# Kernel tuning notes

Measured on AMD Instinct MI355X. Metric: run time of the kernel, lower is better.

Reference implementation:

```python
import jax, jax.numpy as jnp
import numpy as np

B, LQ, D = 4, 10000, 256
HEADS, LVLS, PTS = 8, 1, 4
HW = 100
LIN = HW * HW


def setup_inputs() -> dict:
    key = jax.random.key(0)
    ks = jax.random.split(key, 14)
    s = 0.02
    ctr = jax.random.uniform(ks[2], (B, LQ, LVLS, 2), jnp.float32)
    wh = 0.05 + 0.2 * jax.random.uniform(ks[3], (B, LQ, LVLS, 2), jnp.float32)
    return {
        "query": jax.random.normal(ks[0], (B, LQ, D), jnp.float32),
        "reference_points": jnp.concatenate([ctr, wh], axis=-1),
        "input_flatten": jax.random.normal(ks[1], (B, LIN, D), jnp.float32),
        "input_spatial_shapes": jnp.array([[HW, HW]], jnp.int32),
        "input_level_start_index": jnp.zeros((LVLS,), jnp.int32),
        "input_padding_mask": jnp.zeros((B, LIN), jnp.bool_),
        "Wv": s * jax.random.normal(ks[4], (D, D), jnp.float32),
        "bv": jnp.zeros((D,), jnp.float32),
        "Woff": s * jax.random.normal(ks[5], (D, HEADS * LVLS * PTS * 2), jnp.float32),
        "boff": s * jax.random.normal(ks[6], (HEADS * LVLS * PTS * 2,), jnp.float32),
        "Wa": s * jax.random.normal(ks[7], (D, HEADS * LVLS * PTS), jnp.float32),
        "ba": jnp.zeros((HEADS * LVLS * PTS,), jnp.float32),
        "Wout": s * jax.random.normal(ks[8], (D, D), jnp.float32),
        "bout": jnp.zeros((D,), jnp.float32),
    }


def _ms_deform_attn(query, reference_points, input_flatten, input_padding_mask,
                    Wv, bv, Woff, boff, Wa, ba, Wout, bout):
    Bn, Lq, Dm = query.shape
    Lin = input_flatten.shape[1]
    Hh, L, P = HEADS, LVLS, PTS
    Cd = Dm // Hh
    # value projection + padding mask
    value = input_flatten @ Wv + bv
    value = jnp.where(input_padding_mask[..., None], 0.0, value)
    # sampling offsets & attention weights
    off = (query @ Woff + boff).reshape(Bn, Lq, Hh, L, P, 2)
    attn = jax.nn.softmax((query @ Wa + ba).reshape(Bn, Lq, Hh, L * P), axis=-1)
    loc = (reference_points[:, :, None, :, None, :2]
           + off / P * reference_points[:, :, None, :, None, 2:] * 0.5)
    # value -> (B*Hh, Cd, Lin); square single-level map H=W=sqrt(Lin)
    v = value.reshape(Bn, Lin, Hh, Cd).transpose(0, 2, 3, 1).reshape(Bn * Hh, Cd, Lin)
    Hs = int(round(Lin ** 0.5)); Ws = Hs
    # level 0 grid: (B*Hh, Lq, P, 2), normalized to [-1, 1]
    g = (2.0 * loc - 1.0)[:, :, :, 0].transpose(0, 2, 1, 3, 4).reshape(Bn * Hh, Lq, P, 2)
    x = (g[..., 0] + 1.0) * Ws / 2.0 - 0.5
    y = (g[..., 1] + 1.0) * Hs / 2.0 - 0.5
    x0 = jnp.floor(x).astype(jnp.int32); y0 = jnp.floor(y).astype(jnp.int32)
    x1 = x0 + 1; y1 = y0 + 1
    wx = x - x0.astype(x.dtype); wy = y - y0.astype(y.dtype)

    def valid(xi, yi):
        return ((xi >= 0) & (xi < Ws) & (yi >= 0) & (yi < Hs)).astype(value.dtype)

    def gather(xi, yi):
        idx = (jnp.clip(yi, 0, Hs - 1) * Ws + jnp.clip(xi, 0, Ws - 1)).reshape(Bn * Hh, 1, Lq * P)
        out = jnp.take_along_axis(v, jnp.broadcast_to(idx, (Bn * Hh, Cd, Lq * P)), axis=2)
        return out.reshape(Bn * Hh, Cd, Lq, P)

    sv = (gather(x0, y0) * ((1 - wx) * (1 - wy) * valid(x0, y0))[:, None]
          + gather(x0, y1) * ((1 - wx) * wy * valid(x0, y1))[:, None]
          + gather(x1, y0) * (wx * (1 - wy) * valid(x1, y0))[:, None]
          + gather(x1, y1) * (wx * wy * valid(x1, y1))[:, None])  # (B*Hh, Cd, Lq, P)
    aw = attn.transpose(0, 2, 1, 3).reshape(Bn * Hh, 1, Lq, L * P)
    out = (sv * aw).sum(-1).reshape(Bn, Hh * Cd, Lq).transpose(0, 2, 1)  # (B, Lq, D)
    return out @ Wout + bout


def reference(query, reference_points, input_flatten, input_spatial_shapes,
              input_level_start_index, input_padding_mask,
              Wv, bv, Woff, boff, Wa, ba, Wout, bout):
    # input_spatial_shapes / level_start_index are redundant here: the core is
    # single-level with H=W=sqrt(Len_in) (faithful to the source code).
    return _ms_deform_attn(query, reference_points, input_flatten, input_padding_mask,
                           Wv, bv, Woff, boff, Wa, ba, Wout, bout)
```

## Files before the change

kernel.cpp:

```cpp
#include <hip/hip_runtime.h>

#define BATCH 4
#define LQ    10000
#define DM    256
#define NH    8
#define NP    4
#define HWD   100
#define LIN   10000

typedef unsigned short ushort_t;
typedef __attribute__((ext_vector_type(8))) short bf16x8;
typedef __attribute__((ext_vector_type(8))) unsigned short u16x8;
typedef __attribute__((ext_vector_type(4))) float f32x4;

__device__ __forceinline__ unsigned short f2bf(float f) {
    unsigned int u = __float_as_uint(f);
    u += 0x7FFFu + ((u >> 16) & 1u);
    return (unsigned short)(u >> 16);
}

__device__ __forceinline__ u16x8 pack8(float4 f0, float4 f1) {
    u16x8 pk;
    pk[0] = f2bf(f0.x); pk[1] = f2bf(f0.y);
    pk[2] = f2bf(f0.z); pk[3] = f2bf(f0.w);
    pk[4] = f2bf(f1.x); pk[5] = f2bf(f1.y);
    pk[6] = f2bf(f1.z); pk[7] = f2bf(f1.w);
    return pk;
}

__device__ __forceinline__ void gload16(const ushort_t* g, ushort_t* l) {
    __builtin_amdgcn_global_load_lds(
        (const __attribute__((address_space(1))) void*)g,
        (__attribute__((address_space(3))) void*)l, 16, 0, 0);
}

__global__ __launch_bounds__(256) void prep_kernel(
    const float* __restrict__ Wv, const float* __restrict__ Wout,
    const float* __restrict__ Woff, const float* __restrict__ Wa,
    const float* __restrict__ boff, const float* __restrict__ ba,
    ushort_t* __restrict__ WtV, ushort_t* __restrict__ WtO,
    ushort_t* __restrict__ Wcomb, float* __restrict__ bcomb)
{
    const int n = blockIdx.x, k = threadIdx.x;
    const int t32 = k >> 5, lc = (k >> 3) & 3, j = k & 7;
    const int ct = lc ^ ((n >> 1) & 3);
    const size_t addr = (size_t)n * 256 + t32 * 32 + ct * 8 + j;
    if (blockIdx.y == 0) {
        WtV[addr] = f2bf(Wv[(size_t)k * 256 + n]);
    } else if (blockIdx.y == 1) {
        WtO[addr] = f2bf(Wout[(size_t)k * 256 + n]);
    } else if (n < 96) {
        float w = (n < 64) ? Woff[(size_t)k * 64 + n] : Wa[(size_t)k * 32 + (n - 64)];
        Wcomb[addr] = f2bf(w);
        if (k == 0) bcomb[n] = (n < 64) ? boff[n] : ba[n - 64];
    }
}

__global__ __launch_bounds__(256) void gemm_in_kernel(
    const float* __restrict__ flat, const float* __restrict__ query,
    const ushort_t* __restrict__ WtV, const ushort_t* __restrict__ Wcomb,
    const float* __restrict__ bv, const float* __restrict__ bcomb,
    ushort_t* __restrict__ value, float* __restrict__ oaproj)
{
    __shared__ ushort_t As[2][64 * 32];
    __shared__ ushort_t Bs[2][128 * 32];

    const int tid  = threadIdx.x;
    const int lane = tid & 63;
    const int wv   = tid >> 6;

    const int ar  = tid >> 2;
    const int akb = tid & 3;
    const int asw = (akb ^ ((ar >> 1) & 3)) * 8;
    const int fr = lane & 15, kb = lane >> 4;
    const int ln4 = lane >> 2, lc4 = lane & 3;

    const bool isVal = (blockIdx.x < 1250);
    const int row0 = isVal ? (blockIdx.x >> 1) * 64 : (blockIdx.x - 1250) * 64;
    const int col0 = isVal ? (blockIdx.x & 1) * 128 : 0;
    const float* ap = isVal ? &flat [(size_t)(row0 + ar) * 256 + akb * 8]
                            : &query[(size_t)(row0 + ar) * 256 + akb * 8];
    const ushort_t* Wt = isVal ? WtV : Wcomb;
    const int nrows = isVal ? 128 : 96;

    const f32x4 zero = {0.f, 0.f, 0.f, 0.f};
    f32x4 acc[4][2];
    #pragma unroll
    for (int m = 0; m < 4; ++m)
        #pragma unroll
        for (int n = 0; n < 2; ++n) acc[m][n] = zero;

    {
        float4 f0 = *reinterpret_cast<const float4*>(ap);
        float4 f1 = *reinterpret_cast<const float4*>(ap + 4);
        #pragma unroll
        for (int it = 0; it < 2; ++it) {
            int r0 = (it * 4 + wv) * 16;
            if (r0 < nrows)
                gload16(&Wt[(size_t)(col0 + r0 + ln4) * 256 + lc4 * 8],
                        &Bs[0][r0 * 32]);
        }
        *reinterpret_cast<u16x8*>(&As[0][ar * 32 + asw]) = pack8(f0, f1);
    }
    __syncthreads();

    int c = 0;
    for (int t = 0; t < 8; ++t) {
        const int kn = (t + 1) * 32;
        const bool pf = (t < 7);
        float4 f0, f1;
        if (pf) {
            f0 = *reinterpret_cast<const float4*>(ap + kn);
            f1 = *reinterpret_cast<const float4*>(ap + kn + 4);
            #pragma unroll
            for (int it = 0; it < 2; ++it) {
                int r0 = (it * 4 + wv) * 16;
                if (r0 < nrows)
                    gload16(&Wt[(size_t)(col0 + r0 + ln4) * 256 + kn + lc4 * 8],
                            &Bs[c ^ 1][r0 * 32]);
            }
        }
        bf16x8 af[4], bf[2];
        #pragma unroll
        for (int m = 0; m < 4; ++m) {
            int r = m * 16 + fr;
            af[m] = *reinterpret_cast<const bf16x8*>(
                &As[c][r * 32 + ((kb ^ ((r >> 1) & 3)) * 8)]);
        }
        #pragma unroll
        for (int n = 0; n < 2; ++n) {
            int lr = wv * 32 + n * 16 + fr;
            bf[n] = *reinterpret_cast<const bf16x8*>(
                &Bs[c][lr * 32 + ((kb ^ ((lr >> 1) & 3)) * 8)]);
        }
        #pragma unroll
        for (int m = 0; m < 4; ++m)
            #pragma unroll
            for (int n = 0; n < 2; ++n)
                acc[m][n] = __builtin_amdgcn_mfma_f32_16x16x32_bf16(
                    af[m], bf[n], acc[m][n], 0, 0, 0);
        if (pf)
            *reinterpret_cast<u16x8*>(&As[c ^ 1][ar * 32 + asw]) = pack8(f0, f1);
        __syncthreads();
        c ^= 1;
    }

    if (isVal) {
        #pragma unroll
        for (int n = 0; n < 2; ++n) {
            int cc = col0 + wv * 32 + n * 16 + fr;
            float bb = bv[cc];
            int hh = cc >> 5, ch = cc & 31;
            #pragma unroll
            for (int m = 0; m < 4; ++m) {
                #pragma unroll
                for (int j = 0; j < 4; ++j) {
                    int r = row0 + m * 16 + kb * 4 + j;
                    int rb = (int)((unsigned)r / 10000u);
                    int pix = r - rb * 10000;
                    size_t addr = (((size_t)(rb * 8 + hh)) * LIN + pix) * 32 + ch;
                    value[addr] = f2bf(acc[m][n][j] + bb);
                }
            }
        }
    } else {
        #pragma unroll
        for (int n = 0; n < 2; ++n) {
            int cc = wv * 32 + n * 16 + fr;
            if (cc < 96) {
                float bb = bcomb[cc];
                #pragma unroll
                for (int m = 0; m < 4; ++m) {
                    #pragma unroll
                    for (int j = 0; j < 4; ++j) {
                        int r = row0 + m * 16 + kb * 4 + j;
                        oaproj[(size_t)r * 96 + cc] = acc[m][n][j] + bb;
                    }
                }
            }
        }
    }
}

__global__ __launch_bounds__(256, 4) void deform_kernel(
    const float* __restrict__ oaproj, const float* __restrict__ refpts,
    const ushort_t* __restrict__ value, ushort_t* __restrict__ out)
{
    __shared__ int4   soff[NP * 64];
    __shared__ float4 swt [NP * 64];

    const int blk = blockIdx.x;
    const int xcd = blk & 7;
    const int sub = (blk >> 3) & 3;
    const int chunk = blk >> 5;
    const int map = xcd * 4 + sub;
    const int b = map >> 3, h = map & 7;
    const int q0 = chunk * 64;

    const int tid = threadIdx.x;

    if (tid < 64) {
        const int qg = q0 + tid;
        if (qg >= LQ) {
            int4 zi = {0, 0, 0, 0};
            float4 zf = {0.f, 0.f, 0.f, 0.f};
            #pragma unroll
            for (int p = 0; p < NP; ++p) { soff[p * 64 + tid] = zi; swt[p * 64 + tid] = zf; }
        } else {
            const size_t row = (size_t)b * LQ + qg;
            const float* oa = oaproj + row * 96;
            float4 l4 = *reinterpret_cast<const float4*>(oa + 64 + h * 4);
            float mx = fmaxf(fmaxf(l4.x, l4.y), fmaxf(l4.z, l4.w));
            float e0 = __expf(l4.x - mx), e1 = __expf(l4.y - mx);
            float e2 = __expf(l4.z - mx), e3 = __expf(l4.w - mx);
            float inv = 1.f / (e0 + e1 + e2 + e3);
            float ew[4] = {e0 * inv, e1 * inv, e2 * inv, e3 * inv};
            float4 o0 = *reinterpret_cast<const float4*>(oa + h * 8);
            float4 o1 = *reinterpret_cast<const float4*>(oa + h * 8 + 4);
            float oxv[4] = {o0.x, o0.z, o1.x, o1.z};
            float oyv[4] = {o0.y, o0.w, o1.y, o1.w};
            const float* rp = refpts + row * 4;
            float cx = rp[0], cy = rp[1], rw = rp[2], rh = rp[3];
            #pragma unroll
            for (int p = 0; p < NP; ++p) {
                float x = (cx + oxv[p] * rw * 0.125f) * (float)HWD - 0.5f;
                float y = (cy + oyv[p] * rh * 0.125f) * (float)HWD - 0.5f;
                float x0f = floorf(x), y0f = floorf(y);
                float wx = x - x0f, wy = y - y0f;
                int x0 = (int)x0f, y0 = (int)y0f;
                int x1 = x0 + 1, y1 = y0 + 1;
                float vx0 = (x0 >= 0 && x0 < HWD) ? 1.f : 0.f;
                float vx1 = (x1 >= 0 && x1 < HWD) ? 1.f : 0.f;
                float vy0 = (y0 >= 0 && y0 < HWD) ? 1.f : 0.f;
                float vy1 = (y1 >= 0 && y1 < HWD) ? 1.f : 0.f;
                int cx0 = min(max(x0, 0), HWD - 1), cx1 = min(max(x1, 0), HWD - 1);
                int cy0 = min(max(y0, 0), HWD - 1), cy1 = min(max(y1, 0), HWD - 1);
                float aw = ew[p];
                int4 of = {cy0 * HWD + cx0, cy0 * HWD + cx1,
                           cy1 * HWD + cx0, cy1 * HWD + cx1};
                float4 wt = {aw * (1.f - wx) * (1.f - wy) * vx0 * vy0,
                             aw * wx * (1.f - wy) * vx1 * vy0,
                             aw * (1.f - wx) * wy * vx0 * vy1,
                             aw * wx * wy * vx1 * vy1};
                soff[p * 64 + tid] = of;
                swt [p * 64 + tid] = wt;
            }
        }
    }
    __syncthreads();

    const int q = tid >> 2, c8 = tid & 3;
    const int qg = q0 + q;
    const ushort_t* vb = value + (size_t)map * (LIN * 32) + c8 * 8;

    int4 of[4]; float4 w4[4];
    #pragma unroll
    for (int p = 0; p < NP; ++p) {
        of[p] = soff[p * 64 + q];
        w4[p] = swt [p * 64 + q];
    }
    uint4 vv[4][4];
    #pragma unroll
    for (int p = 0; p < NP; ++p) {
        vv[p][0] = *reinterpret_cast<const uint4*>(vb + ((size_t)of[p].x << 5));
        vv[p][1] = *reinterpret_cast<const uint4*>(vb + ((size_t)of[p].y << 5));
        vv[p][2] = *reinterpret_cast<const uint4*>(vb + ((size_t)of[p].z << 5));
        vv[p][3] = *reinterpret_cast<const uint4*>(vb + ((size_t)of[p].w << 5));
    }
    float a0 = 0.f, a1 = 0.f, a2 = 0.f, a3 = 0.f;
    float a4 = 0.f, a5 = 0.f, a6 = 0.f, a7 = 0.f;
    #define ACC(V, W) { const float w_ = (W); const uint4 v_ = (V); \
        a0 += w_ * __uint_as_float(v_.x << 16); \
        a1 += w_ * __uint_as_float(v_.x & 0xffff0000u); \
        a2 += w_ * __uint_as_float(v_.y << 16); \
        a3 += w_ * __uint_as_float(v_.y & 0xffff0000u); \
        a4 += w_ * __uint_as_float(v_.z << 16); \
        a5 += w_ * __uint_as_float(v_.z & 0xffff0000u); \
        a6 += w_ * __uint_as_float(v_.w << 16); \
        a7 += w_ * __uint_as_float(v_.w & 0xffff0000u); }
    #pragma unroll
    for (int p = 0; p < NP; ++p) {
        ACC(vv[p][0], w4[p].x);
        ACC(vv[p][1], w4[p].y);
        ACC(vv[p][2], w4[p].z);
        ACC(vv[p][3], w4[p].w);
    }
    #undef ACC

    if (qg < LQ) {
        const size_t orow = (size_t)b * LQ + qg;
        u16x8 pk;
        pk[0] = f2bf(a0); pk[1] = f2bf(a1);
        pk[2] = f2bf(a2); pk[3] = f2bf(a3);
        pk[4] = f2bf(a4); pk[5] = f2bf(a5);
        pk[6] = f2bf(a6); pk[7] = f2bf(a7);
        const int cc = h * 4 + c8;
        const int t32 = cc >> 2;
        const int ct = (cc & 3) ^ ((int)(orow >> 1) & 3);
        *reinterpret_cast<u16x8*>(&out[orow * 256 + t32 * 32 + ct * 8]) = pk;
    }
}

__global__ __launch_bounds__(256) void gemm_out_kernel(
    const ushort_t* __restrict__ A, const ushort_t* __restrict__ Wt,
    const float* __restrict__ bias, float* __restrict__ Cout)
{
    __shared__ ushort_t As[2][64 * 32];
    __shared__ ushort_t Bs[2][128 * 32];

    const int tid  = threadIdx.x;
    const int lane = tid & 63;
    const int wv   = tid >> 6;
    const int row0 = (blockIdx.x >> 1) * 64;
    const int col0 = (blockIdx.x & 1) * 128;

    const f32x4 zero = {0.f, 0.f, 0.f, 0.f};
    f32x4 acc[4][2];
    #pragma unroll
    for (int m = 0; m < 4; ++m)
        #pragma unroll
        for (int n = 0; n < 2; ++n) acc[m][n] = zero;

    const int fr = lane & 15, kb = lane >> 4;
    const int ln4 = lane >> 2, lc4 = lane & 3;

    {
        gload16(&A[(size_t)(row0 + wv * 16 + ln4) * 256 + lc4 * 8],
                &As[0][wv * 512]);
        #pragma unroll
        for (int it = 0; it < 2; ++it) {
            int r0 = (it * 4 + wv) * 16;
            gload16(&Wt[(size_t)(col0 + r0 + ln4) * 256 + lc4 * 8], &Bs[0][r0 * 32]);
        }
    }
    __syncthreads();

    int c = 0;
    for (int t = 0; t < 8; ++t) {
        const int kn = (t + 1) * 32;
        if (t < 7) {
            gload16(&A[(size_t)(row0 + wv * 16 + ln4) * 256 + kn + lc4 * 8],
                    &As[c ^ 1][wv * 512]);
            #pragma unroll
            for (int it = 0; it < 2; ++it) {
                int r0 = (it * 4 + wv) * 16;
                gload16(&Wt[(size_t)(col0 + r0 + ln4) * 256 + kn + lc4 * 8],
                        &Bs[c ^ 1][r0 * 32]);
            }
        }
        bf16x8 af[4], bf[2];
        #pragma unroll
        for (int m = 0; m < 4; ++m) {
            int r = m * 16 + fr;
            af[m] = *reinterpret_cast<const bf16x8*>(
                &As[c][r * 32 + ((kb ^ ((r >> 1) & 3)) * 8)]);
        }
        #pragma unroll
        for (int n = 0; n < 2; ++n) {
            int lr = wv * 32 + n * 16 + fr;
            bf[n] = *reinterpret_cast<const bf16x8*>(
                &Bs[c][lr * 32 + ((kb ^ ((lr >> 1) & 3)) * 8)]);
        }
        #pragma unroll
        for (int m = 0; m < 4; ++m)
            #pragma unroll
            for (int n = 0; n < 2; ++n)
                acc[m][n] = __builtin_amdgcn_mfma_f32_16x16x32_bf16(
                    af[m], bf[n], acc[m][n], 0, 0, 0);
        __syncthreads();
        c ^= 1;
    }

    #pragma unroll
    for (int m = 0; m < 4; ++m) {
        #pragma unroll
        for (int n = 0; n < 2; ++n) {
            int cc = col0 + wv * 32 + n * 16 + fr;
            float bb = bias[cc];
            #pragma unroll
            for (int j = 0; j < 4; ++j) {
                int r = row0 + m * 16 + kb * 4 + j;
                Cout[(size_t)r * 256 + cc] = acc[m][n][j] + bb;
            }
        }
    }
}

extern "C" void kernel_launch(void* const* d_in, const int* in_sizes, int n_in,
                              void* d_out, int out_size, void* d_ws, size_t ws_size,
                              hipStream_t stream)
{
    const float* query  = (const float*)d_in[0];
    const float* refpts = (const float*)d_in[1];
    const float* flat   = (const float*)d_in[2];
    const float* Wv   = (const float*)d_in[6];
    const float* bv   = (const float*)d_in[7];
    const float* Woff = (const float*)d_in[8];
    const float* boff = (const float*)d_in[9];
    const float* Wa   = (const float*)d_in[10];
    const float* ba   = (const float*)d_in[11];
    const float* Wout = (const float*)d_in[12];
    const float* bout = (const float*)d_in[13];
    float* out = (float*)d_out;

    const size_t MROWS = (size_t)BATCH * LIN;
    ushort_t* value  = (ushort_t*)d_ws;
    ushort_t* ws2    = value + MROWS * DM;
    ushort_t* WtV    = ws2 + MROWS * DM;
    ushort_t* WtO    = WtV + 256 * 256;
    ushort_t* Wcomb  = WtO + 256 * 256;
    float*    bcomb  = (float*)(Wcomb + 96 * 256);
    float*    oaproj = bcomb + 128;

    dim3 blk(256);

    prep_kernel<<<dim3(256, 3), blk, 0, stream>>>(
        Wv, Wout, Woff, Wa, boff, ba, WtV, WtO, Wcomb, bcomb);

    gemm_in_kernel<<<dim3(1875), blk, 0, stream>>>(
        flat, query, WtV, Wcomb, bv, bcomb, value, oaproj);

    deform_kernel<<<dim3(157 * 32), blk, 0, stream>>>(
        oaproj, refpts, value, ws2);

    gemm_out_kernel<<<dim3(1250), blk, 0, stream>>>(
        ws2, WtO, bout, out);
}
```

Measured before the change: 78.76 us.

## Use full-width N tiles in input and output GEMMs to avoid re-reading A

Both GEMM kernels now compute all 256 output columns per block instead of splitting N across two blocks. The input GEMM uses 32-row tiles with half the threads staging the fp32 A rows, and the output GEMM keeps 64 rows with a 4x4 MFMA tile per wave. This avoids loading and converting the fp32 activations twice and halves the redundant A traffic. The cost is more LDS for weights and more accumulator registers, which may lower occupancy.

```diff
diff --git a/kernel.cpp b/kernel.cpp
--- a/kernel.cpp
+++ b/kernel.cpp
@@ -56,51 +56,53 @@
     }
 }
 
-__global__ __launch_bounds__(256) void gemm_in_kernel(
+__global__ __launch_bounds__(256, 4) void gemm_in_kernel(
     const float* __restrict__ flat, const float* __restrict__ query,
     const ushort_t* __restrict__ WtV, const ushort_t* __restrict__ Wcomb,
     const float* __restrict__ bv, const float* __restrict__ bcomb,
     ushort_t* __restrict__ value, float* __restrict__ oaproj)
 {
-    __shared__ ushort_t As[2][64 * 32];
-    __shared__ ushort_t Bs[2][128 * 32];
+    __shared__ ushort_t As[2][32 * 32];
+    __shared__ ushort_t Bs[2][256 * 32];
 
     const int tid  = threadIdx.x;
     const int lane = tid & 63;
     const int wv   = tid >> 6;
 
-    const int ar  = tid >> 2;
+    const int ar  = (tid >> 2) & 31;
     const int akb = tid & 3;
     const int asw = (akb ^ ((ar >> 1) & 3)) * 8;
     const int fr = lane & 15, kb = lane >> 4;
     const int ln4 = lane >> 2, lc4 = lane & 3;
 
     const bool isVal = (blockIdx.x < 1250);
-    const int row0 = isVal ? (blockIdx.x >> 1) * 64 : (blockIdx.x - 1250) * 64;
-    const int col0 = isVal ? (blockIdx.x & 1) * 128 : 0;
-    const float* ap = isVal ? &flat [(size_t)(row0 + ar) * 256 + akb * 8]
-                            : &query[(size_t)(row0 + ar) * 256 + akb * 8];
+    const int row0 = (isVal ? blockIdx.x : (blockIdx.x - 1250)) * 32;
+    const float* Abase = isVal ? flat : query;
     const ushort_t* Wt = isVal ? WtV : Wcomb;
-    const int nrows = isVal ? 128 : 96;
+    const int nrows = isVal ? 256 : 96;
+
+    const float* ap = &Abase[(size_t)(row0 + ar) * 256 + akb * 8];
+    const bool aStager = (tid < 128);
 
     const f32x4 zero = {0.f, 0.f, 0.f, 0.f};
-    f32x4 acc[4][2];
-    #pragma unroll
-    for (int m = 0; m < 4; ++m)
-        #pragma unroll
-        for (int n = 0; n < 2; ++n) acc[m][n] = zero;
+    f32x4 acc[2][4];
+    #pragma unroll
+    for (int m = 0; m < 2; ++m)
+        #pragma unroll
+        for (int n = 0; n < 4; ++n) acc[m][n] = zero;
 
     {
-        float4 f0 = *reinterpret_cast<const float4*>(ap);
-        float4 f1 = *reinterpret_cast<const float4*>(ap + 4);
-        #pragma unroll
-        for (int it = 0; it < 2; ++it) {
+        #pragma unroll
+        for (int it = 0; it < 4; ++it) {
             int r0 = (it * 4 + wv) * 16;
             if (r0 < nrows)
-                gload16(&Wt[(size_t)(col0 + r0 + ln4) * 256 + lc4 * 8],
-                        &Bs[0][r0 * 32]);
-        }
-        *reinterpret_cast<u16x8*>(&As[0][ar * 32 + asw]) = pack8(f0, f1);
+                gload16(&Wt[(size_t)(r0 + ln4) * 256 + lc4 * 8], &Bs[0][r0 * 32]);
+        }
+        if (aStager) {
+            float4 f0 = *reinterpret_cast<const float4*>(ap);
+            float4 f1 = *reinterpret_cast<const float4*>(ap + 4);
+            *reinterpret_cast<u16x8*>(&As[0][ar * 32 + asw]) = pack8(f0, f1);
+        }
     }
     __syncthreads();
 
@@ -110,36 +112,38 @@
         const bool pf = (t < 7);
         float4 f0, f1;
         if (pf) {
-            f0 = *reinterpret_cast<const float4*>(ap + kn);
-            f1 = *reinterpret_cast<const float4*>(ap + kn + 4);
-            #pragma unroll
-            for (int it = 0; it < 2; ++it) {
+            if (aStager) {
+                f0 = *reinterpret_cast<const float4*>(ap + kn);
+                f1 = *reinterpret_cast<const float4*>(ap + kn + 4);
+            }
+            #pragma unroll
+            for (int it = 0; it < 4; ++it) {
                 int r0 = (it * 4 + wv) * 16;
                 if (r0 < nrows)
-                    gload16(&Wt[(size_t)(col0 + r0 + ln4) * 256 + kn + lc4 * 8],
+                    gload16(&Wt[(size_t)(r0 + ln4) * 256 + kn + lc4 * 8],
                             &Bs[c ^ 1][r0 * 32]);
             }
         }
-        bf16x8 af[4], bf[2];
-        #pragma unroll
-        for (int m = 0; m < 4; ++m) {
+        bf16x8 af[2], bf[4];
+        #pragma unroll
+        for (int m = 0; m < 2; ++m) {
             int r = m * 16 + fr;
             af[m] = *reinterpret_cast<const bf16x8*>(
                 &As[c][r * 32 + ((kb ^ ((r >> 1) & 3)) * 8)]);
         }
         #pragma unroll
-        for (int n = 0; n < 2; ++n) {
-            int lr = wv * 32 + n * 16 + fr;
+        for (int n = 0; n < 4; ++n) {
+            int cc = wv * 64 + n * 16 + fr;
             bf[n] = *reinterpret_cast<const bf16x8*>(
-                &Bs[c][lr * 32 + ((kb ^ ((lr >> 1) & 3)) * 8)]);
-        }
-        #pragma unroll
-        for (int m = 0; m < 4; ++m)
-            #pragma unroll
-            for (int n = 0; n < 2; ++n)
+                &Bs[c][cc * 32 + ((kb ^ ((cc >> 1) & 3)) * 8)]);
+        }
+        #pragma unroll
+        for (int m = 0; m < 2; ++m)
+            #pragma unroll
+            for (int n = 0; n < 4; ++n)
                 acc[m][n] = __builtin_amdgcn_mfma_f32_16x16x32_bf16(
                     af[m], bf[n], acc[m][n], 0, 0, 0);
-        if (pf)
+        if (pf && aStager)
             *reinterpret_cast<u16x8*>(&As[c ^ 1][ar * 32 + asw]) = pack8(f0, f1);
         __syncthreads();
         c ^= 1;
@@ -147,12 +151,12 @@
 
     if (isVal) {
         #pragma unroll
-        for (int n = 0; n < 2; ++n) {
-            int cc = col0 + wv * 32 + n * 16 + fr;
+        for (int n = 0; n < 4; ++n) {
+            int cc = wv * 64 + n * 16 + fr;
             float bb = bv[cc];
             int hh = cc >> 5, ch = cc & 31;
             #pragma unroll
-            for (int m = 0; m < 4; ++m) {
+            for (int m = 0; m < 2; ++m) {
                 #pragma unroll
                 for (int j = 0; j < 4; ++j) {
                     int r = row0 + m * 16 + kb * 4 + j;
@@ -165,12 +169,12 @@
         }
     } else {
         #pragma unroll
-        for (int n = 0; n < 2; ++n) {
-            int cc = wv * 32 + n * 16 + fr;
+        for (int n = 0; n < 4; ++n) {
+            int cc = wv * 64 + n * 16 + fr;
             if (cc < 96) {
                 float bb = bcomb[cc];
                 #pragma unroll
-                for (int m = 0; m < 4; ++m) {
+                for (int m = 0; m < 2; ++m) {
                     #pragma unroll
                     for (int j = 0; j < 4; ++j) {
                         int r = row0 + m * 16 + kb * 4 + j;
@@ -306,20 +310,19 @@
     const float* __restrict__ bias, float* __restrict__ Cout)
 {
     __shared__ ushort_t As[2][64 * 32];
-    __shared__ ushort_t Bs[2][128 * 32];
+    __shared__ ushort_t Bs[2][256 * 32];
 
     const int tid  = threadIdx.x;
     const int lane = tid & 63;
     const int wv   = tid >> 6;
-    const int row0 = (blockIdx.x >> 1) * 64;
-    const int col0 = (blockIdx.x & 1) * 128;
+    const int row0 = blockIdx.x * 64;
 
     const f32x4 zero = {0.f, 0.f, 0.f, 0.f};
-    f32x4 acc[4][2];
+    f32x4 acc[4][4];
     #pragma unroll
     for (int m = 0; m < 4; ++m)
         #pragma unroll
-        for (int n = 0; n < 2; ++n) acc[m][n] = zero;
+        for (int n = 0; n < 4; ++n) acc[m][n] = zero;
 
     const int fr = lane & 15, kb = lane >> 4;
     const int ln4 = lane >> 2, lc4 = lane & 3;
@@ -328,9 +331,9 @@
         gload16(&A[(size_t)(row0 + wv * 16 + ln4) * 256 + lc4 * 8],
                 &As[0][wv * 512]);
         #pragma unroll
-        for (int it = 0; it < 2; ++it) {
+        for (int it = 0; it < 4; ++it) {
             int r0 = (it * 4 + wv) * 16;
-            gload16(&Wt[(size_t)(col0 + r0 + ln4) * 256 + lc4 * 8], &Bs[0][r0 * 32]);
+            gload16(&Wt[(size_t)(r0 + ln4) * 256 + lc4 * 8], &Bs[0][r0 * 32]);
         }
     }
     __syncthreads();
@@ -342,13 +345,13 @@
             gload16(&A[(size_t)(row0 + wv * 16 + ln4) * 256 + kn + lc4 * 8],
                     &As[c ^ 1][wv * 512]);
             #pragma unroll
-            for (int it = 0; it < 2; ++it) {
+            for (int it = 0; it < 4; ++it) {
                 int r0 = (it * 4 + wv) * 16;
-                gload16(&Wt[(size_t)(col0 + r0 + ln4) * 256 + kn + lc4 * 8],
+                gload16(&Wt[(size_t)(r0 + ln4) * 256 + kn + lc4 * 8],
                         &Bs[c ^ 1][r0 * 32]);
             }
         }
-        bf16x8 af[4], bf[2];
+        bf16x8 af[4], bf[4];
         #pragma unroll
         for (int m = 0; m < 4; ++m) {
             int r = m * 16 + fr;
@@ -356,15 +359,15 @@
                 &As[c][r * 32 + ((kb ^ ((r >> 1) & 3)) * 8)]);
         }
         #pragma unroll
-        for (int n = 0; n < 2; ++n) {
-            int lr = wv * 32 + n * 16 + fr;
+        for (int n = 0; n < 4; ++n) {
+            int cc = wv * 64 + n * 16 + fr;
             bf[n] = *reinterpret_cast<const bf16x8*>(
-                &Bs[c][lr * 32 + ((kb ^ ((lr >> 1) & 3)) * 8)]);
+                &Bs[c][cc * 32 + ((kb ^ ((cc >> 1) & 3)) * 8)]);
         }
         #pragma unroll
         for (int m = 0; m < 4; ++m)
             #pragma unroll
-            for (int n = 0; n < 2; ++n)
+            for (int n = 0; n < 4; ++n)
                 acc[m][n] = __builtin_amdgcn_mfma_f32_16x16x32_bf16(
                     af[m], bf[n], acc[m][n], 0, 0, 0);
         __syncthreads();
@@ -374,8 +377,8 @@
     #pragma unroll
     for (int m = 0; m < 4; ++m) {
         #pragma unroll
-        for (int n = 0; n < 2; ++n) {
-            int cc = col0 + wv * 32 + n * 16 + fr;
+        for (int n = 0; n < 4; ++n) {
+            int cc = wv * 64 + n * 16 + fr;
             float bb = bias[cc];
             #pragma unroll
             for (int j = 0; j < 4; ++j) {
@@ -417,12 +420,12 @@
     prep_kernel<<<dim3(256, 3), blk, 0, stream>>>(
         Wv, Wout, Woff, Wa, boff, ba, WtV, WtO, Wcomb, bcomb);
 
-    gemm_in_kernel<<<dim3(1875), blk, 0, stream>>>(
+    gemm_in_kernel<<<dim3(2500), blk, 0, stream>>>(
         flat, query, WtV, Wcomb, bv, bcomb, value, oaproj);
 
     deform_kernel<<<dim3(157 * 32), blk, 0, stream>>>(
         oaproj, refpts, value, ws2);
 
-    gemm_out_kernel<<<dim3(1250), blk, 0, stream>>>(
+    gemm_out_kernel<<<dim3(MROWS / 64), blk, 0, stream>>>(
         ws2, WtO, bout, out);
 }
```

After: 75.58 us. 4.0% less time.
